# Kernel optimization log

Measured on AMD Instinct MI355X. Metric: run time of the kernel, lower is better.

The kernel has to match this reference:

```python
import jax, jax.numpy as jnp
import numpy as np

NC = 6          # num_classes
RM = 16         # reg_max
TOPK = 10       # tal_topk
IMG = 640.0
STRIDES = (8, 16, 32)
BS = 32
NGT = 20        # GT boxes per image (uniform -> static max_boxes)


def _iou(b1, b2, ciou, eps=1e-7):
    x1 = jnp.maximum(b1[..., 0], b2[..., 0]); y1 = jnp.maximum(b1[..., 1], b2[..., 1])
    x2 = jnp.minimum(b1[..., 2], b2[..., 2]); y2 = jnp.minimum(b1[..., 3], b2[..., 3])
    inter = jnp.maximum(x2 - x1, 0.0) * jnp.maximum(y2 - y1, 0.0)
    w1 = jnp.maximum(b1[..., 2] - b1[..., 0], eps); h1 = jnp.maximum(b1[..., 3] - b1[..., 1], eps)
    w2 = jnp.maximum(b2[..., 2] - b2[..., 0], eps); h2 = jnp.maximum(b2[..., 3] - b2[..., 1], eps)
    union = w1 * h1 + w2 * h2 - inter + eps
    iou = inter / union
    if not ciou:
        return iou
    cw = jnp.maximum(b1[..., 2], b2[..., 2]) - jnp.minimum(b1[..., 0], b2[..., 0])
    ch = jnp.maximum(b1[..., 3], b2[..., 3]) - jnp.minimum(b1[..., 1], b2[..., 1])
    c2 = cw ** 2 + ch ** 2 + eps
    rho2 = ((b1[..., 0] + b1[..., 2] - b2[..., 0] - b2[..., 2]) ** 2
            + (b1[..., 1] + b1[..., 3] - b2[..., 1] - b2[..., 3]) ** 2) / 4.0
    v = (4.0 / (np.pi ** 2)) * (jnp.arctan(w2 / h2) - jnp.arctan(w1 / h1)) ** 2
    alpha = jax.lax.stop_gradient(v / (v - iou + (1.0 + eps)))
    return iou - (rho2 / c2 + v * alpha)


def _forward(p0, p1, p2, targets):
    bs = p0.shape[0]
    regs, clss, ancs, strs = [], [], [], []
    for p, s in zip((p0, p1, p2), STRIDES):
        b, c, h, w = p.shape
        p = jnp.transpose(p, (0, 2, 3, 1)).reshape(b, h * w, c)
        regs.append(p[..., :4 * RM].reshape(b, h * w, 4, RM))
        clss.append(p[..., 4 * RM:])
        gy, gx = jnp.meshgrid(jnp.arange(h), jnp.arange(w), indexing='ij')
        ancs.append(((jnp.stack([gx, gy], -1).astype(jnp.float32) + 0.5) * s).reshape(-1, 2))
        strs.append(jnp.full((h * w, 1), float(s), jnp.float32))
    pred_reg = jnp.concatenate(regs, 1)      # [bs, A, 4, RM]
    pred_cls = jnp.concatenate(clss, 1)      # [bs, A, NC]
    anchors = jnp.concatenate(ancs, 0)       # [A, 2] pixel coords
    stride_a = jnp.concatenate(strs, 0)      # [A, 1]
    A = anchors.shape[0]

    proj = jnp.arange(RM, dtype=jnp.float32)
    pd_dist = jnp.sum(jax.nn.softmax(pred_reg, -1) * proj, -1)       # [bs, A, 4]
    anc_b = jnp.broadcast_to(anchors[None], (bs, A, 2))
    pd_boxes = jnp.concatenate([anc_b - pd_dist[..., :2] * stride_a,
                                anc_b + pd_dist[..., 2:] * stride_a], -1)

    # GT parse: exactly NGT rows per image, grouped by image index (static reshape)
    G = targets.shape[0] // bs
    t = targets.reshape(bs, G, 6)
    gt_labels = t[..., 1]
    xywh = t[..., 2:6] * IMG
    gt_boxes = jnp.concatenate([xywh[..., :2] - xywh[..., 2:] / 2,
                                xywh[..., :2] + xywh[..., 2:] / 2], -1)  # [bs, G, 4]
    mask_gt = jnp.ones((bs, G, 1), jnp.float32)

    # ---- task-aligned assignment (on detached preds) ----
    pscore = jax.nn.sigmoid(jax.lax.stop_gradient(pred_cls))
    pbox_d = jax.lax.stop_gradient(pd_boxes)
    ious = _iou(gt_boxes[:, :, None, :], pbox_d[:, None, :, :], False)   # [bs, G, A]
    labels_i = gt_labels.astype(jnp.int32)
    scores = jnp.einsum('bac,bgc->bga', pscore, jax.nn.one_hot(labels_i, NC, dtype=pscore.dtype))
    align = (scores ** 0.5) * (ious ** 6.0)
    lt = anc_b[:, None, :, :] - gt_boxes[:, :, None, :2]
    rb = gt_boxes[:, :, None, 2:] - anc_b[:, None, :, :]
    in_gts = jnp.min(jnp.concatenate([lt, rb], -1), -1) > 1e-9
    align = align * in_gts * mask_gt
    _, tk_idx = jax.lax.top_k(align, TOPK)
    bi = jnp.arange(bs)[:, None, None]; gi = jnp.arange(G)[None, :, None]
    mask_pos = jnp.zeros((bs, G, A), bool).at[bi, gi, tk_idx].set(True)
    mask_pos = mask_pos & (align > 0)
    multi = jnp.sum(mask_pos, 1) > 1                                   # [bs, A]
    full = jnp.moveaxis(jax.nn.one_hot(jnp.argmax(align, 1), G), -1, 1) > 0.5
    mask_pos = jnp.where(multi[:, None, :], full, mask_pos)

    fg = jnp.any(mask_pos, 1)                                          # [bs, A]
    gt_idx = jnp.argmax(mask_pos, 1)                                   # [bs, A] (first True)
    tb = jnp.take_along_axis(gt_boxes, jnp.broadcast_to(gt_idx[..., None], (bs, A, 4)), axis=1)
    target_boxes = jnp.where(fg[..., None], tb, 0.0)
    t_lab = jnp.take_along_axis(labels_i, gt_idx, axis=1)
    iou_fg = jnp.maximum(jax.lax.stop_gradient(_iou(pd_boxes, target_boxes, False)), 0.0)
    norm_align = align / (jnp.max(align, -1, keepdims=True) + 1e-9)
    norm_g = jnp.take_along_axis(norm_align, gt_idx[:, None, :], axis=1)[:, 0, :]
    sval = jnp.where(fg, norm_g * iou_fg, 0.0)
    target_scores = sval[..., None] * jax.nn.one_hot(t_lab, NC, dtype=jnp.float32)

    # cls: BCE with logits, sum / num_anchors
    x = pred_cls
    bce = jnp.maximum(x, 0.0) - x * target_scores + jnp.log1p(jnp.exp(-jnp.abs(x)))
    loss_cls = jnp.sum(bce) / float(A)

    fgf = fg.astype(jnp.float32)
    num_pos = jnp.maximum(jnp.sum(fgf), 1.0)

    # bbox: 1 - CIoU over positives
    ciou = _iou(pd_boxes, target_boxes, True)
    loss_bbox = jnp.sum((1.0 - ciou) * fgf) / num_pos

    # DFL
    ltrb = jnp.concatenate([(anc_b - target_boxes[..., :2]) / stride_a,
                            (target_boxes[..., 2:] - anc_b) / stride_a], -1)
    ltrb = jnp.clip(ltrb, 0.0, RM - 1.01)
    tl = ltrb.astype(jnp.int32)
    wl = (tl + 1).astype(jnp.float32) - ltrb
    wr = ltrb - tl.astype(jnp.float32)
    logZ = jax.nn.logsumexp(pred_reg, -1)                              # [bs, A, 4]
    ce_l = logZ - jnp.take_along_axis(pred_reg, tl[..., None], -1)[..., 0]
    ce_r = logZ - jnp.take_along_axis(pred_reg, (tl + 1)[..., None], -1)[..., 0]
    loss_dfl = jnp.sum(jnp.sum(ce_l * wl + ce_r * wr, -1) * fgf) / num_pos

    l_cls = loss_cls * 1.0
    l_bbox = loss_bbox * 7.5
    l_dfl = loss_dfl * 1.5
    return jnp.stack([l_cls + l_bbox + l_dfl, l_cls, l_bbox, jnp.asarray(0.0, jnp.float32), l_dfl])


def setup_inputs() -> dict:
    key = jax.random.key(0)
    k0, k1, k2, k3, k4, k5 = jax.random.split(key, 6)
    C = 4 * RM + NC
    p0 = jax.random.normal(k0, (BS, C, 80, 80), jnp.float32)
    p1 = jax.random.normal(k1, (BS, C, 40, 40), jnp.float32)
    p2 = jax.random.normal(k2, (BS, C, 20, 20), jnp.float32)
    bidx = jnp.repeat(jnp.arange(BS), NGT).astype(jnp.float32)
    lab = jax.random.randint(k3, (BS * NGT,), 0, NC).astype(jnp.float32)
    cxcy = jax.random.uniform(k4, (BS * NGT, 2), minval=0.2, maxval=0.8)
    wh = jax.random.uniform(k5, (BS * NGT, 2), minval=0.05, maxval=0.3)
    targets = jnp.concatenate([bidx[:, None], lab[:, None], cxcy, wh], 1)
    return {"p0": p0, "p1": p1, "p2": p2, "targets": targets}


def reference(p0, p1, p2, targets):
    return _forward(p0, p1, p2, targets)
```

## Files before the change

### kernel.cpp

```cpp
#include <hip/hip_runtime.h>
#include <math.h>

#define NC 6
#define RM 16
#define TOPK 10
#define BSZ 32
#define G 20
#define A_TOT 8400
#define NBA (BSZ * A_TOT)
#define NBLK_PREP (NBA / 256)
#define NBLK_LOSS ((NBA + 255) / 256)
#define MAXCAND 1024

__device__ __forceinline__ void anchor_decode(int a, int& lvl, int& ai, int& w, int& hw, float& s) {
    if (a < 6400)      { lvl = 0; ai = a;        w = 80; hw = 6400; s = 8.f; }
    else if (a < 8000) { lvl = 1; ai = a - 6400; w = 40; hw = 1600; s = 16.f; }
    else               { lvl = 2; ai = a - 8000; w = 20; hw = 400;  s = 32.f; }
}

__device__ __forceinline__ float align_from(const float* __restrict__ trow, float logit,
                                            float4 box, float ax, float ay) {
    float cx = trow[2] * 640.f, cy = trow[3] * 640.f;
    float hwd = trow[4] * 320.f, hh = trow[5] * 320.f;
    float gx1 = cx - hwd, gy1 = cy - hh, gx2 = cx + hwd, gy2 = cy + hh;
    float mn = fminf(fminf(ax - gx1, ay - gy1), fminf(gx2 - ax, gy2 - ay));
    if (mn <= 1e-9f) return 0.f;
    const float eps = 1e-7f;
    float x1 = fmaxf(gx1, box.x), y1 = fmaxf(gy1, box.y);
    float x2 = fminf(gx2, box.z), y2 = fminf(gy2, box.w);
    float inter = fmaxf(x2 - x1, 0.f) * fmaxf(y2 - y1, 0.f);
    float gw = fmaxf(gx2 - gx1, eps), gh = fmaxf(gy2 - gy1, eps);
    float w2 = fmaxf(box.z - box.x, eps), h2 = fmaxf(box.w - box.y, eps);
    float uni = gw * gh + w2 * h2 - inter + eps;
    float iou = inter / uni;
    float sc = 1.f / (1.f + __expf(-logit));
    float i2 = iou * iou;
    return sqrtf(sc) * (i2 * i2 * i2);
}

__global__ __launch_bounds__(256) void k_prep(
        const float* __restrict__ p0, const float* __restrict__ p1, const float* __restrict__ p2,
        float* __restrict__ pd_boxes, float* __restrict__ logZ,
        unsigned int* __restrict__ mask, float* __restrict__ partial_prep) {
    __shared__ float sdist[256 * 4];
    __shared__ float slz[256 * 4];
    int tid = blockIdx.x * 256 + threadIdx.x;
    int q = tid >> 2;
    int sd = tid & 3;
    int idx4 = q * 4;
    int b = idx4 / A_TOT, a4 = idx4 % A_TOT;
    int lvl, ai, w, hw; float s;
    anchor_decode(a4, lvl, ai, w, hw, s);
    const float* p = (lvl == 0) ? p0 : ((lvl == 1) ? p1 : p2);
    const float* base = p + (size_t)b * 70 * hw + ai;

    float4 se = make_float4(0, 0, 0, 0), sk = make_float4(0, 0, 0, 0);
    #pragma unroll
    for (int k = 0; k < RM; ++k) {
        float4 v = *(const float4*)(base + (size_t)(sd * RM + k) * hw);
        float fk = (float)k;
        float ex = __expf(v.x); se.x += ex; sk.x += ex * fk;
        float ey = __expf(v.y); se.y += ey; sk.y += ey * fk;
        float ez = __expf(v.z); se.z += ez; sk.z += ez * fk;
        float ew = __expf(v.w); se.w += ew; sk.w += ew * fk;
    }
    ((float4*)sdist)[threadIdx.x] =
        make_float4(sk.x / se.x, sk.y / se.y, sk.z / se.z, sk.w / se.w);
    ((float4*)slz)[threadIdx.x] =
        make_float4(__logf(se.x), __logf(se.y), __logf(se.z), __logf(se.w));

    float bce = 0.f;
    {
        float4 x = *(const float4*)(base + (size_t)(64 + sd) * hw);
        bce += fmaxf(x.x, 0.f) + __logf(1.f + __expf(-fabsf(x.x)));
        bce += fmaxf(x.y, 0.f) + __logf(1.f + __expf(-fabsf(x.y)));
        bce += fmaxf(x.z, 0.f) + __logf(1.f + __expf(-fabsf(x.z)));
        bce += fmaxf(x.w, 0.f) + __logf(1.f + __expf(-fabsf(x.w)));
        if (sd < 2) {
            float4 y = *(const float4*)(base + (size_t)(68 + sd) * hw);
            bce += fmaxf(y.x, 0.f) + __logf(1.f + __expf(-fabsf(y.x)));
            bce += fmaxf(y.y, 0.f) + __logf(1.f + __expf(-fabsf(y.y)));
            bce += fmaxf(y.z, 0.f) + __logf(1.f + __expf(-fabsf(y.z)));
            bce += fmaxf(y.w, 0.f) + __logf(1.f + __expf(-fabsf(y.w)));
        }
    }
    mask[tid] = 0u;
    __syncthreads();

    int gb = (threadIdx.x & ~3) * 4;
    float d0 = sdist[gb + sd], d1 = sdist[gb + 4 + sd];
    float d2 = sdist[gb + 8 + sd], d3 = sdist[gb + 12 + sd];
    float z0 = slz[gb + sd], z1 = slz[gb + 4 + sd];
    float z2 = slz[gb + 8 + sd], z3 = slz[gb + 12 + sd];
    float ax = ((float)(ai % w + sd) + 0.5f) * s;
    float ay = ((float)(ai / w) + 0.5f) * s;
    ((float4*)pd_boxes)[tid] = make_float4(ax - d0 * s, ay - d1 * s, ax + d2 * s, ay + d3 * s);
    ((float4*)logZ)[tid] = make_float4(z0, z1, z2, z3);

    __shared__ float part[4];
    int lane = threadIdx.x & 63, wv = threadIdx.x >> 6;
    #pragma unroll
    for (int off = 32; off > 0; off >>= 1) bce += __shfl_down(bce, off);
    if (lane == 0) part[wv] = bce;
    __syncthreads();
    if (threadIdx.x == 0)
        partial_prep[blockIdx.x] = part[0] + part[1] + part[2] + part[3];
}

__device__ __forceinline__ bool cand_better(float av, int ai_, float bv, int bi_) {
    if (av > bv) return true;
    if (av < bv) return false;
    if (ai_ < 0) return false;
    if (bi_ < 0) return true;
    return ai_ < bi_;
}

__global__ __launch_bounds__(256) void k_align(
        const float* __restrict__ targets,
        const float* __restrict__ pd_boxes,
        const float* __restrict__ p0, const float* __restrict__ p1, const float* __restrict__ p2,
        float* __restrict__ amax, unsigned int* __restrict__ mask) {
    __shared__ float cval[MAXCAND];
    __shared__ int   cidx[MAXCAND];
    __shared__ int   cnt_s;
    __shared__ float rv[4];
    __shared__ int   ri[4];
    __shared__ int   win_i_s;

    int bg = blockIdx.x;
    int b = bg / G;
    int g = bg % G;
    const float* t = targets + (size_t)bg * 6;
    int lab = (int)t[1];
    const float* cb[3];
    cb[0] = p0 + (size_t)b * 70 * 6400 + (size_t)(64 + lab) * 6400;
    cb[1] = p1 + (size_t)b * 70 * 1600 + (size_t)(64 + lab) * 1600;
    cb[2] = p2 + (size_t)b * 70 * 400  + (size_t)(64 + lab) * 400;
    const float4* pb = (const float4*)pd_boxes + (size_t)b * A_TOT;

    float cx = t[2] * 640.f, cy = t[3] * 640.f;
    float hwd = t[4] * 320.f, hh = t[5] * 320.f;
    float gx1 = cx - hwd, gy1 = cy - hh, gx2 = cx + hwd, gy2 = cy + hh;

    const float sv3[3] = {8.f, 16.f, 32.f};
    const int   wv3[3] = {80, 40, 20};
    const int   ov3[3] = {0, 6400, 8000};
    int x0[3], y0[3], nx[3], ncell[3];
    int ntot = 0;
    #pragma unroll
    for (int l = 0; l < 3; ++l) {
        float s = sv3[l]; int w = wv3[l];
        int xa = max(0, (int)floorf(gx1 / s - 0.5f));
        int xb = min(w - 1, (int)ceilf(gx2 / s - 0.5f));
        int ya = max(0, (int)floorf(gy1 / s - 0.5f));
        int yb = min(w - 1, (int)ceilf(gy2 / s - 0.5f));
        x0[l] = xa; y0[l] = ya;
        nx[l] = max(0, xb - xa + 1);
        int nyl = max(0, yb - ya + 1);
        ncell[l] = nx[l] * nyl;
        ntot += ncell[l];
    }

    if (threadIdx.x == 0) cnt_s = 0;
    __syncthreads();

    for (int i = threadIdx.x; i < ntot; i += 256) {
        int l = 0, loc = i;
        if (loc >= ncell[0]) { loc -= ncell[0]; l = 1; }
        if (l == 1 && loc >= ncell[1]) { loc -= ncell[1]; l = 2; }
        int iy = loc / nx[l], ix = loc % nx[l];
        ix += x0[l]; iy += y0[l];
        float s = sv3[l]; int w = wv3[l];
        float ax = ((float)ix + 0.5f) * s, ay = ((float)iy + 0.5f) * s;
        int a = ov3[l] + iy * w + ix;
        float logit = cb[l][iy * w + ix];
        float al = align_from(t, logit, pb[a], ax, ay);
        if (al > 0.f) {
            int p = atomicAdd(&cnt_s, 1);
            if (p < MAXCAND) { cval[p] = al; cidx[p] = a; }
        }
    }
    __syncthreads();
    int cnt = min(cnt_s, MAXCAND);

    float mv[MAXCAND / 256];
    int   mi[MAXCAND / 256];
    #pragma unroll
    for (int r = 0; r < MAXCAND / 256; ++r) {
        int p = threadIdx.x + r * 256;
        mv[r] = (p < cnt) ? cval[p] : -1.f;
        mi[r] = (p < cnt) ? cidx[p] : -1;
    }

    int lane = threadIdx.x & 63, wv = threadIdx.x >> 6;
    for (int it = 0; it < TOPK; ++it) {
        float v = -1.f; int vi = -1;
        #pragma unroll
        for (int r = 0; r < MAXCAND / 256; ++r)
            if (cand_better(mv[r], mi[r], v, vi)) { v = mv[r]; vi = mi[r]; }
        #pragma unroll
        for (int off = 32; off > 0; off >>= 1) {
            float ov = __shfl_down(v, off);
            int   oi = __shfl_down(vi, off);
            if (cand_better(ov, oi, v, vi)) { v = ov; vi = oi; }
        }
        if (lane == 0) { rv[wv] = v; ri[wv] = vi; }
        __syncthreads();
        if (threadIdx.x == 0) {
            float v0 = rv[0]; int i0 = ri[0];
            for (int i = 1; i < 4; ++i)
                if (cand_better(rv[i], ri[i], v0, i0)) { v0 = rv[i]; i0 = ri[i]; }
            if (it == 0) amax[bg] = fmaxf(v0, 0.f);
            if (i0 >= 0 && v0 > 0.f) atomicOr(&mask[(size_t)b * A_TOT + i0], 1u << g);
            win_i_s = i0;
        }
        __syncthreads();
        int wi = win_i_s;
        if (wi < 0) break;
        #pragma unroll
        for (int r = 0; r < MAXCAND / 256; ++r)
            if (mi[r] == wi) { mv[r] = -1.f; mi[r] = -1; }
    }
}

__global__ __launch_bounds__(256) void k_loss(
        const float* __restrict__ targets,
        const float* __restrict__ pd_boxes, const float* __restrict__ logZ,
        const float* __restrict__ amax, const unsigned int* __restrict__ mask,
        const float* __restrict__ p0, const float* __restrict__ p1, const float* __restrict__ p2,
        float* __restrict__ partial) {
    int idx = blockIdx.x * 256 + threadIdx.x;
    float bce_s = 0.f, bbox_s = 0.f, dfl_s = 0.f, fg_s = 0.f;
    if (idx < NBA) {
        unsigned int m = mask[idx];
        if (m != 0u) {
            int b = idx / A_TOT, a = idx % A_TOT;
            int lvl, ai, w_, hw; float s;
            anchor_decode(a, lvl, ai, w_, hw, s);
            const float* p = (lvl == 0) ? p0 : ((lvl == 1) ? p1 : p2);
            const float* base = p + (size_t)b * 70 * hw + ai;
            float ax = ((ai % w_) + 0.5f) * s, ay = ((ai / w_) + 0.5f) * s;
            float4 box = ((const float4*)pd_boxes)[idx];
            int gidx;
            if (__popc(m) > 1) {
                float best = -1.f; gidx = 0;
                for (int g = 0; g < G; ++g) {
                    const float* tg = targets + ((size_t)b * G + g) * 6;
                    int labg = (int)tg[1];
                    float al = align_from(tg, base[(size_t)(64 + labg) * hw], box, ax, ay);
                    if (al > best) { best = al; gidx = g; }
                }
            } else {
                gidx = __ffs(m) - 1;
            }
            const float* t = targets + ((size_t)b * G + gidx) * 6;
            int lab = (int)t[1];
            float logit = base[(size_t)(64 + lab) * hw];
            float al = align_from(t, logit, box, ax, ay);
            float cx = t[2] * 640.f, cy = t[3] * 640.f;
            float hwd = t[4] * 320.f, hh = t[5] * 320.f;
            float tbx1 = cx - hwd, tby1 = cy - hh, tbx2 = cx + hwd, tby2 = cy + hh;
            const float eps = 1e-7f;
            float x1 = fmaxf(box.x, tbx1), y1 = fmaxf(box.y, tby1);
            float x2 = fminf(box.z, tbx2), y2 = fminf(box.w, tby2);
            float inter = fmaxf(x2 - x1, 0.f) * fmaxf(y2 - y1, 0.f);
            float w1 = fmaxf(box.z - box.x, eps), h1 = fmaxf(box.w - box.y, eps);
            float w2 = fmaxf(tbx2 - tbx1, eps), h2 = fmaxf(tby2 - tby1, eps);
            float uni = w1 * h1 + w2 * h2 - inter + eps;
            float iou = inter / uni;
            float iou_fg = fmaxf(iou, 0.f);
            float sval = (al / (amax[b * G + gidx] + 1e-9f)) * iou_fg;
            bce_s = -logit * sval;
            fg_s = 1.f;
            float cw = fmaxf(box.z, tbx2) - fminf(box.x, tbx1);
            float ch = fmaxf(box.w, tby2) - fminf(box.y, tby1);
            float c2 = cw * cw + ch * ch + eps;
            float dx = box.x + box.z - tbx1 - tbx2;
            float dy = box.y + box.w - tby1 - tby2;
            float rho2 = (dx * dx + dy * dy) * 0.25f;
            float dv = atanf(w2 / h2) - atanf(w1 / h1);
            float v = 0.40528473f * dv * dv;
            float alpha = v / (v - iou + (1.f + eps));
            float ciou = iou - (rho2 / c2 + v * alpha);
            bbox_s = 1.f - ciou;
            float4 lzv = ((const float4*)logZ)[idx];
            float lz[4] = {lzv.x, lzv.y, lzv.z, lzv.w};
            float lt[4] = {(ax - tbx1) / s, (ay - tby1) / s, (tbx2 - ax) / s, (tby2 - ay) / s};
            #pragma unroll
            for (int sd = 0; sd < 4; ++sd) {
                float d = fminf(fmaxf(lt[sd], 0.f), (float)RM - 1.01f);
                int tl = (int)d;
                float wl = (float)(tl + 1) - d;
                float wr = d - (float)tl;
                float xl = base[(size_t)(sd * RM + tl) * hw];
                float xr = base[(size_t)(sd * RM + tl + 1) * hw];
                dfl_s += (lz[sd] - xl) * wl + (lz[sd] - xr) * wr;
            }
        }
    }
    __shared__ float part[4][4];
    int lane = threadIdx.x & 63, wv = threadIdx.x >> 6;
    #pragma unroll
    for (int off = 32; off > 0; off >>= 1) {
        bce_s  += __shfl_down(bce_s,  off);
        bbox_s += __shfl_down(bbox_s, off);
        dfl_s  += __shfl_down(dfl_s,  off);
        fg_s   += __shfl_down(fg_s,   off);
    }
    if (lane == 0) {
        part[wv][0] = bce_s; part[wv][1] = bbox_s;
        part[wv][2] = dfl_s; part[wv][3] = fg_s;
    }
    __syncthreads();
    if (threadIdx.x == 0) {
        float s0 = 0.f, s1 = 0.f, s2 = 0.f, s3 = 0.f;
        for (int i = 0; i < 4; ++i) {
            s0 += part[i][0]; s1 += part[i][1]; s2 += part[i][2]; s3 += part[i][3];
        }
        ((float4*)partial)[blockIdx.x] = make_float4(s0, s1, s2, s3);
    }
}

__global__ __launch_bounds__(256) void k_final(const float* __restrict__ partial,
                                               const float* __restrict__ partial_prep,
                                               float* __restrict__ out) {
    double s0 = 0., s1 = 0., s2 = 0., s3 = 0.;
    for (int i = threadIdx.x; i < NBLK_LOSS; i += 256) {
        float4 p = ((const float4*)partial)[i];
        s0 += p.x; s1 += p.y; s2 += p.z; s3 += p.w;
    }
    for (int i = threadIdx.x; i < NBLK_PREP; i += 256)
        s0 += partial_prep[i];
    #pragma unroll
    for (int off = 32; off > 0; off >>= 1) {
        s0 += __shfl_down(s0, off);
        s1 += __shfl_down(s1, off);
        s2 += __shfl_down(s2, off);
        s3 += __shfl_down(s3, off);
    }
    __shared__ double part[4][4];
    int lane = threadIdx.x & 63, wv = threadIdx.x >> 6;
    if (lane == 0) { part[wv][0] = s0; part[wv][1] = s1; part[wv][2] = s2; part[wv][3] = s3; }
    __syncthreads();
    if (threadIdx.x == 0) {
        double bce = 0., bbox = 0., dfl = 0., fgc = 0.;
        for (int i = 0; i < 4; ++i) {
            bce += part[i][0]; bbox += part[i][1]; dfl += part[i][2]; fgc += part[i][3];
        }
        double l_cls = bce / (double)A_TOT;
        double np_ = fmax(fgc, 1.0);
        double l_bbox = 7.5 * bbox / np_;
        double l_dfl = 1.5 * dfl / np_;
        out[0] = (float)(l_cls + l_bbox + l_dfl);
        out[1] = (float)l_cls;
        out[2] = (float)l_bbox;
        out[3] = 0.f;
        out[4] = (float)l_dfl;
    }
}

extern "C" void kernel_launch(void* const* d_in, const int* in_sizes, int n_in,
                              void* d_out, int out_size, void* d_ws, size_t ws_size,
                              hipStream_t stream) {
    const float* p0 = (const float*)d_in[0];
    const float* p1 = (const float*)d_in[1];
    const float* p2 = (const float*)d_in[2];
    const float* targets = (const float*)d_in[3];
    float* out = (float*)d_out;

    char* ws = (char*)d_ws;
    size_t off = 0;
    float* pd_boxes = (float*)(ws + off); off += (size_t)NBA * 4 * sizeof(float);
    float* logZ     = (float*)(ws + off); off += (size_t)NBA * 4 * sizeof(float);
    float* amax     = (float*)(ws + off); off += (size_t)BSZ * G * sizeof(float);
    unsigned int* mask = (unsigned int*)(ws + off); off += (size_t)NBA * sizeof(unsigned int);
    float* partial  = (float*)(ws + off); off += (size_t)NBLK_LOSS * 4 * sizeof(float);
    float* partial_prep = (float*)(ws + off); off += (size_t)NBLK_PREP * sizeof(float);

    k_prep<<<NBLK_PREP, 256, 0, stream>>>(p0, p1, p2, pd_boxes, logZ, mask, partial_prep);
    k_align<<<BSZ * G, 256, 0, stream>>>(targets, pd_boxes, p0, p1, p2, amax, mask);
    k_loss<<<NBLK_LOSS, 256, 0, stream>>>(targets, pd_boxes, logZ, amax, mask,
                                          p0, p1, p2, partial);
    k_final<<<1, 256, 0, stream>>>(partial, partial_prep, out);
}
```

Measured before the change: 143.0 us.

## Replace LDS transpose with shuffles, wave-local top-k, fuse final reduction

In k_prep, the per-anchor distances and log-sums are now transposed across lanes with xor shuffles instead of through shared memory and a block barrier. In k_align, the block max is computed once during candidate collection, and each wave extracts its own top-k before wave 0 merges them, removing two block barriers per top-k iteration. The separate k_final launch is folded into k_loss using a last-block-done atomic counter. Together these cut synchronisation and one kernel launch, at the cost of extra shuffle work and a threadfence/atomic handshake.

```diff
diff --git a/kernel.cpp b/kernel.cpp
--- a/kernel.cpp
+++ b/kernel.cpp
@@ -41,9 +41,8 @@
 __global__ __launch_bounds__(256) void k_prep(
         const float* __restrict__ p0, const float* __restrict__ p1, const float* __restrict__ p2,
         float* __restrict__ pd_boxes, float* __restrict__ logZ,
-        unsigned int* __restrict__ mask, float* __restrict__ partial_prep) {
-    __shared__ float sdist[256 * 4];
-    __shared__ float slz[256 * 4];
+        unsigned int* __restrict__ mask, float* __restrict__ partial_prep,
+        unsigned int* __restrict__ done) {
     int tid = blockIdx.x * 256 + threadIdx.x;
     int q = tid >> 2;
     int sd = tid & 3;
@@ -64,10 +63,25 @@
         float ez = __expf(v.z); se.z += ez; sk.z += ez * fk;
         float ew = __expf(v.w); se.w += ew; sk.w += ew * fk;
     }
-    ((float4*)sdist)[threadIdx.x] =
-        make_float4(sk.x / se.x, sk.y / se.y, sk.z / se.z, sk.w / se.w);
-    ((float4*)slz)[threadIdx.x] =
-        make_float4(__logf(se.x), __logf(se.y), __logf(se.z), __logf(se.w));
+    float d0 = sk.x / se.x, d1 = sk.y / se.y, d2 = sk.z / se.z, d3 = sk.w / se.w;
+    float z0 = __logf(se.x), z1 = __logf(se.y), z2 = __logf(se.z), z3 = __logf(se.w);
+
+    bool lo = (sd & 1) == 0, hi = (sd & 2) == 0;
+    float ea0 = __shfl_xor(d0, 1), ea1 = __shfl_xor(d1, 1), ea2 = __shfl_xor(d2, 1), ea3 = __shfl_xor(d3, 1);
+    float na0 = lo ? d0 : ea1, na1 = lo ? ea0 : d1, na2 = lo ? d2 : ea3, na3 = lo ? ea2 : d3;
+    float fa0 = __shfl_xor(na0, 2), fa1 = __shfl_xor(na1, 2), fa2 = __shfl_xor(na2, 2), fa3 = __shfl_xor(na3, 2);
+    float ma0 = hi ? na0 : fa2, ma1 = hi ? na1 : fa3, ma2 = hi ? fa0 : na2, ma3 = hi ? fa1 : na3;
+    float za0 = __shfl_xor(z0, 1), za1 = __shfl_xor(z1, 1), za2 = __shfl_xor(z2, 1), za3 = __shfl_xor(z3, 1);
+    float zb0 = lo ? z0 : za1, zb1 = lo ? za0 : z1, zb2 = lo ? z2 : za3, zb3 = lo ? za2 : z3;
+    float zc0 = __shfl_xor(zb0, 2), zc1 = __shfl_xor(zb1, 2), zc2 = __shfl_xor(zb2, 2), zc3 = __shfl_xor(zb3, 2);
+    float zd0 = hi ? zb0 : zc2, zd1 = hi ? zb1 : zc3, zd2 = hi ? zc0 : zb2, zd3 = hi ? zc1 : zb3;
+
+    float ax = ((float)(ai % w + sd) + 0.5f) * s;
+    float ay = ((float)(ai / w) + 0.5f) * s;
+    ((float4*)pd_boxes)[tid] = make_float4(ax - ma0 * s, ay - ma1 * s, ax + ma2 * s, ay + ma3 * s);
+    ((float4*)logZ)[tid] = make_float4(zd0, zd1, zd2, zd3);
+    mask[tid] = 0u;
+    if (tid == 0) *done = 0u;
 
     float bce = 0.f;
     {
@@ -84,18 +98,6 @@
             bce += fmaxf(y.w, 0.f) + __logf(1.f + __expf(-fabsf(y.w)));
         }
     }
-    mask[tid] = 0u;
-    __syncthreads();
-
-    int gb = (threadIdx.x & ~3) * 4;
-    float d0 = sdist[gb + sd], d1 = sdist[gb + 4 + sd];
-    float d2 = sdist[gb + 8 + sd], d3 = sdist[gb + 12 + sd];
-    float z0 = slz[gb + sd], z1 = slz[gb + 4 + sd];
-    float z2 = slz[gb + 8 + sd], z3 = slz[gb + 12 + sd];
-    float ax = ((float)(ai % w + sd) + 0.5f) * s;
-    float ay = ((float)(ai / w) + 0.5f) * s;
-    ((float4*)pd_boxes)[tid] = make_float4(ax - d0 * s, ay - d1 * s, ax + d2 * s, ay + d3 * s);
-    ((float4*)logZ)[tid] = make_float4(z0, z1, z2, z3);
 
     __shared__ float part[4];
     int lane = threadIdx.x & 63, wv = threadIdx.x >> 6;
@@ -123,9 +125,9 @@
     __shared__ float cval[MAXCAND];
     __shared__ int   cidx[MAXCAND];
     __shared__ int   cnt_s;
-    __shared__ float rv[4];
-    __shared__ int   ri[4];
-    __shared__ int   win_i_s;
+    __shared__ float wtv[4][TOPK];
+    __shared__ int   wti[4][TOPK];
+    __shared__ float redf[4];
 
     int bg = blockIdx.x;
     int b = bg / G;
@@ -164,6 +166,7 @@
     if (threadIdx.x == 0) cnt_s = 0;
     __syncthreads();
 
+    float lmax = -1.f;
     for (int i = threadIdx.x; i < ntot; i += 256) {
         int l = 0, loc = i;
         if (loc >= ncell[0]) { loc -= ncell[0]; l = 1; }
@@ -176,13 +179,20 @@
         float logit = cb[l][iy * w + ix];
         float al = align_from(t, logit, pb[a], ax, ay);
         if (al > 0.f) {
+            lmax = fmaxf(lmax, al);
             int p = atomicAdd(&cnt_s, 1);
             if (p < MAXCAND) { cval[p] = al; cidx[p] = a; }
         }
     }
-    __syncthreads();
+    int lane = threadIdx.x & 63, wv = threadIdx.x >> 6;
+    #pragma unroll
+    for (int off = 32; off > 0; off >>= 1) lmax = fmaxf(lmax, __shfl_xor(lmax, off));
+    if (lane == 0) redf[wv] = lmax;
+    __syncthreads();
+    if (threadIdx.x == 0)
+        amax[bg] = fmaxf(fmaxf(fmaxf(redf[0], redf[1]), fmaxf(redf[2], redf[3])), 0.f);
+
     int cnt = min(cnt_s, MAXCAND);
-
     float mv[MAXCAND / 256];
     int   mi[MAXCAND / 256];
     #pragma unroll
@@ -192,34 +202,45 @@
         mi[r] = (p < cnt) ? cidx[p] : -1;
     }
 
-    int lane = threadIdx.x & 63, wv = threadIdx.x >> 6;
     for (int it = 0; it < TOPK; ++it) {
         float v = -1.f; int vi = -1;
         #pragma unroll
         for (int r = 0; r < MAXCAND / 256; ++r)
             if (cand_better(mv[r], mi[r], v, vi)) { v = mv[r]; vi = mi[r]; }
         #pragma unroll
-        for (int off = 32; off > 0; off >>= 1) {
-            float ov = __shfl_down(v, off);
-            int   oi = __shfl_down(vi, off);
+        for (int off = 1; off < 64; off <<= 1) {
+            float ov = __shfl_xor(v, off);
+            int   oi = __shfl_xor(vi, off);
             if (cand_better(ov, oi, v, vi)) { v = ov; vi = oi; }
         }
-        if (lane == 0) { rv[wv] = v; ri[wv] = vi; }
-        __syncthreads();
-        if (threadIdx.x == 0) {
-            float v0 = rv[0]; int i0 = ri[0];
-            for (int i = 1; i < 4; ++i)
-                if (cand_better(rv[i], ri[i], v0, i0)) { v0 = rv[i]; i0 = ri[i]; }
-            if (it == 0) amax[bg] = fmaxf(v0, 0.f);
-            if (i0 >= 0 && v0 > 0.f) atomicOr(&mask[(size_t)b * A_TOT + i0], 1u << g);
-            win_i_s = i0;
-        }
-        __syncthreads();
-        int wi = win_i_s;
-        if (wi < 0) break;
+        if (vi < 0) {
+            if (lane == 0)
+                for (int j = it; j < TOPK; ++j) { wtv[wv][j] = -1.f; wti[wv][j] = -1; }
+            break;
+        }
+        if (lane == 0) { wtv[wv][it] = v; wti[wv][it] = vi; }
         #pragma unroll
         for (int r = 0; r < MAXCAND / 256; ++r)
-            if (mi[r] == wi) { mv[r] = -1.f; mi[r] = -1; }
+            if (mi[r] == vi) { mv[r] = -1.f; mi[r] = -1; }
+    }
+    __syncthreads();
+
+    if (wv == 0) {
+        float v4 = -1.f; int i4 = -1;
+        if (lane < 4 * TOPK) { v4 = wtv[lane / TOPK][lane % TOPK]; i4 = wti[lane / TOPK][lane % TOPK]; }
+        unsigned int* mrow = mask + (size_t)b * A_TOT;
+        for (int it = 0; it < TOPK; ++it) {
+            float v = v4; int vi = i4;
+            #pragma unroll
+            for (int off = 1; off < 64; off <<= 1) {
+                float ov = __shfl_xor(v, off);
+                int   oi = __shfl_xor(vi, off);
+                if (cand_better(ov, oi, v, vi)) { v = ov; vi = oi; }
+            }
+            if (vi < 0) break;
+            if (lane == 0) atomicOr(&mrow[vi], 1u << g);
+            if (i4 == vi) { v4 = -1.f; i4 = -1; }
+        }
     }
 }
 
@@ -228,7 +249,8 @@
         const float* __restrict__ pd_boxes, const float* __restrict__ logZ,
         const float* __restrict__ amax, const unsigned int* __restrict__ mask,
         const float* __restrict__ p0, const float* __restrict__ p1, const float* __restrict__ p2,
-        float* __restrict__ partial) {
+        float* __restrict__ partial, const float* __restrict__ partial_prep,
+        unsigned int* __restrict__ done, float* __restrict__ out) {
     int idx = blockIdx.x * 256 + threadIdx.x;
     float bce_s = 0.f, bbox_s = 0.f, dfl_s = 0.f, fg_s = 0.f;
     if (idx < NBA) {
@@ -319,33 +341,39 @@
         }
         ((float4*)partial)[blockIdx.x] = make_float4(s0, s1, s2, s3);
     }
-}
-
-__global__ __launch_bounds__(256) void k_final(const float* __restrict__ partial,
-                                               const float* __restrict__ partial_prep,
-                                               float* __restrict__ out) {
-    double s0 = 0., s1 = 0., s2 = 0., s3 = 0.;
+
+    __shared__ int amlast;
+    if (threadIdx.x == 0) {
+        __threadfence();
+        unsigned int old = atomicAdd(done, 1u);
+        amlast = (old == (unsigned int)(NBLK_LOSS - 1));
+    }
+    __syncthreads();
+    if (!amlast) return;
+    if (threadIdx.x == 0) *done = 0u;
+    __threadfence();
+
+    double a0 = 0., a1 = 0., a2 = 0., a3 = 0.;
     for (int i = threadIdx.x; i < NBLK_LOSS; i += 256) {
-        float4 p = ((const float4*)partial)[i];
-        s0 += p.x; s1 += p.y; s2 += p.z; s3 += p.w;
+        float4 pp = ((const float4*)partial)[i];
+        a0 += pp.x; a1 += pp.y; a2 += pp.z; a3 += pp.w;
     }
     for (int i = threadIdx.x; i < NBLK_PREP; i += 256)
-        s0 += partial_prep[i];
+        a0 += partial_prep[i];
     #pragma unroll
     for (int off = 32; off > 0; off >>= 1) {
-        s0 += __shfl_down(s0, off);
-        s1 += __shfl_down(s1, off);
-        s2 += __shfl_down(s2, off);
-        s3 += __shfl_down(s3, off);
-    }
-    __shared__ double part[4][4];
-    int lane = threadIdx.x & 63, wv = threadIdx.x >> 6;
-    if (lane == 0) { part[wv][0] = s0; part[wv][1] = s1; part[wv][2] = s2; part[wv][3] = s3; }
+        a0 += __shfl_down(a0, off);
+        a1 += __shfl_down(a1, off);
+        a2 += __shfl_down(a2, off);
+        a3 += __shfl_down(a3, off);
+    }
+    __shared__ double dpart[4][4];
+    if (lane == 0) { dpart[wv][0] = a0; dpart[wv][1] = a1; dpart[wv][2] = a2; dpart[wv][3] = a3; }
     __syncthreads();
     if (threadIdx.x == 0) {
         double bce = 0., bbox = 0., dfl = 0., fgc = 0.;
         for (int i = 0; i < 4; ++i) {
-            bce += part[i][0]; bbox += part[i][1]; dfl += part[i][2]; fgc += part[i][3];
+            bce += dpart[i][0]; bbox += dpart[i][1]; dfl += dpart[i][2]; fgc += dpart[i][3];
         }
         double l_cls = bce / (double)A_TOT;
         double np_ = fmax(fgc, 1.0);
@@ -376,10 +404,10 @@
     unsigned int* mask = (unsigned int*)(ws + off); off += (size_t)NBA * sizeof(unsigned int);
     float* partial  = (float*)(ws + off); off += (size_t)NBLK_LOSS * 4 * sizeof(float);
     float* partial_prep = (float*)(ws + off); off += (size_t)NBLK_PREP * sizeof(float);
-
-    k_prep<<<NBLK_PREP, 256, 0, stream>>>(p0, p1, p2, pd_boxes, logZ, mask, partial_prep);
+    unsigned int* done = (unsigned int*)(ws + off); off += sizeof(unsigned int);
+
+    k_prep<<<NBLK_PREP, 256, 0, stream>>>(p0, p1, p2, pd_boxes, logZ, mask, partial_prep, done);
     k_align<<<BSZ * G, 256, 0, stream>>>(targets, pd_boxes, p0, p1, p2, amax, mask);
     k_loss<<<NBLK_LOSS, 256, 0, stream>>>(targets, pd_boxes, logZ, amax, mask,
-                                          p0, p1, p2, partial);
-    k_final<<<1, 256, 0, stream>>>(partial, partial_prep, out);
-}
+                                          p0, p1, p2, partial, partial_prep, done, out);
+}
```

Result: slower. 161.2 us (+12.7%).
